# Performance work log

Measured on AMD Instinct MI355X. Metric: run time of the kernel, lower is better.

The kernel has to match this reference:

```python
import jax, jax.numpy as jnp
import numpy as np

EMB = 128
EA = 32
ET = 32
N = 50000
E = 500000
EPS = 1e-5
DROP_P = 0.1


def setup_inputs() -> dict:
    key = jax.random.key(0)
    ks = jax.random.split(key, 12)
    din = EMB + EA + ET
    return {
        "hidden": jax.random.normal(ks[0], (N, EMB), jnp.float32),
        "edge_index": jax.random.randint(ks[1], (2, E), 0, N, jnp.int64 if jax.config.jax_enable_x64 else jnp.int32),
        "edge_attr": jax.random.normal(ks[2], (E, EA), jnp.float32),
        "edge_time_emb": jax.random.normal(ks[3], (E, ET), jnp.float32),
        "boundary_condition": jax.random.normal(ks[4], (N, EMB), jnp.float32),
        # learned params (torch Linear stored transposed: [in, out])
        "W_msg": jax.random.normal(ks[5], (din, EMB), jnp.float32) / np.sqrt(din),
        "b_msg": jnp.zeros((EMB,), jnp.float32),
        "W_lin": jax.random.normal(ks[6], (EMB, EMB), jnp.float32) / np.sqrt(EMB),
        "b_lin": jnp.zeros((EMB,), jnp.float32),
        "ln_gamma": jnp.ones((EMB,), jnp.float32),
        "ln_beta": jnp.zeros((EMB,), jnp.float32),
    }


def reference(hidden, edge_index, edge_attr, edge_time_emb, boundary_condition,
              W_msg, b_msg, W_lin, b_lin, ln_gamma, ln_beta):
    num_nodes = hidden.shape[0]
    # gather source node features, concat with edge features -> [E, emb+ea+et]
    msg = jnp.concatenate([hidden[edge_index[0]], edge_attr, edge_time_emb], axis=1)
    msg = jax.nn.relu(msg @ W_msg + b_msg)                      # [E, emb]
    # append boundary condition as self-loop messages
    msg_aug = jnp.concatenate([msg, boundary_condition], axis=0)
    idx_aug = jnp.concatenate([edge_index[1], jnp.arange(num_nodes, dtype=edge_index.dtype)])
    out = jax.ops.segment_sum(msg_aug, idx_aug, num_segments=num_nodes)  # scatter-sum [N, emb]
    out = out @ W_lin + b_lin
    # LayerNorm (eps=1e-5, affine)
    mean = out.mean(-1, keepdims=True)
    var = out.var(-1, keepdims=True)
    out = (out - mean) * jax.lax.rsqrt(var + EPS) * ln_gamma + ln_beta
    out = jax.nn.relu(out)
    # dropout p=0.1, training=True (fixed key for reproducibility)
    keep = jax.random.bernoulli(jax.random.key(42), 1.0 - DROP_P, out.shape)
    out = jnp.where(keep, out / (1.0 - DROP_P), 0.0)
    return out
```

## Files before the change

### kernel.cpp

```cpp
#include <hip/hip_runtime.h>
#include <stdint.h>

#define NN 50000
#define NE 500000
#define SPB 32
#define NEB (NE / SPB)
#define NT_BLOCKS ((NN + 63) / 64)
#define DEG_STRIDE (NT_BLOCKS * 256)
#define NBLK_N ((NN + 255) / 256)

typedef short bf16x8 __attribute__((ext_vector_type(8)));
typedef float f32x4 __attribute__((ext_vector_type(4)));
typedef unsigned short u16;
typedef unsigned short u16x4 __attribute__((ext_vector_type(4)));
typedef unsigned short u16x8 __attribute__((ext_vector_type(8)));
typedef unsigned int u32x2 __attribute__((ext_vector_type(2)));
typedef unsigned int u32x4 __attribute__((ext_vector_type(4)));

__device__ __forceinline__ u16 f2b(float x) {
  uint32_t u = __builtin_bit_cast(uint32_t, x);
  return (u16)((u + 0x7fffu + ((u >> 16) & 1u)) >> 16);
}
__device__ __forceinline__ float b2f(uint32_t lo16) {
  return __builtin_bit_cast(float, lo16 << 16);
}

__device__ __forceinline__ void threefry(uint32_t x0, uint32_t x1,
                                         uint32_t& o0, uint32_t& o1) {
  const uint32_t k0 = 0u, k1 = 42u, k2 = 0u ^ 42u ^ 0x1BD11BDAu;
  x0 += k0; x1 += k1;
#define TFR(r) { x0 += x1; x1 = (x1 << r) | (x1 >> (32 - r)); x1 ^= x0; }
  TFR(13) TFR(15) TFR(26) TFR(6)
  x0 += k1; x1 += k2 + 1u;
  TFR(17) TFR(29) TFR(16) TFR(24)
  x0 += k2; x1 += k0 + 2u;
  TFR(13) TFR(15) TFR(26) TFR(6)
  x0 += k0; x1 += k1 + 3u;
  TFR(17) TFR(29) TFR(16) TFR(24)
  x0 += k1; x1 += k2 + 4u;
  TFR(13) TFR(15) TFR(26) TFR(6)
  x0 += k2; x1 += k0 + 5u;
#undef TFR
  o0 = x0; o1 = x1;
}

__device__ __forceinline__ bool jax_keep(uint32_t j) {
  uint32_t o0, o1;
  threefry(0u, j, o0, o1);
  uint32_t bits = o0 ^ o1;
  float u = __builtin_bit_cast(float, (bits >> 9) | 0x3f800000u) - 1.0f;
  return u < 0.9f;
}

__global__ __launch_bounds__(256) void k_prep(const float* __restrict__ Wmsg,
                                              const float* __restrict__ Wlin,
                                              u16* __restrict__ WhImg,
                                              u16* __restrict__ WcImg,
                                              u16* __restrict__ WlImg,
                                              uint32_t* __restrict__ deg) {
  const int t = threadIdx.x, b = blockIdx.x;
  if (b == 0) {
#pragma unroll
    for (int it = 0; it < 16; ++it) {
      int g = t + (it << 8);
      int d = g >> 5, k4 = (g & 31) << 2;
      u16x4 v = {f2b(Wmsg[(k4 + 0) * 128 + d]), f2b(Wmsg[(k4 + 1) * 128 + d]),
                 f2b(Wmsg[(k4 + 2) * 128 + d]), f2b(Wmsg[(k4 + 3) * 128 + d])};
      *(u16x4*)&WhImg[(d << 7) + k4] = v;
    }
  } else if (b == 1) {
#pragma unroll
    for (int it = 0; it < 8; ++it) {
      int g = t + (it << 8);
      int d = g >> 4, k4 = (g & 15) << 2;
      u16x4 v = {f2b(Wmsg[(128 + k4 + 0) * 128 + d]), f2b(Wmsg[(128 + k4 + 1) * 128 + d]),
                 f2b(Wmsg[(128 + k4 + 2) * 128 + d]), f2b(Wmsg[(128 + k4 + 3) * 128 + d])};
      *(u16x4*)&WcImg[(d << 6) + k4] = v;
    }
  } else if (b == 2) {
#pragma unroll
    for (int it = 0; it < 16; ++it) {
      int g = t + (it << 8);
      int d = g >> 5, k4 = (g & 31) << 2;
      u16x4 v = {f2b(Wlin[(k4 + 0) * 128 + d]), f2b(Wlin[(k4 + 1) * 128 + d]),
                 f2b(Wlin[(k4 + 2) * 128 + d]), f2b(Wlin[(k4 + 3) * 128 + d])};
      *(u16x4*)&WlImg[(d << 7) + k4] = v;
    }
  } else {
    for (int i = ((b - 3) << 8) + t; i < NN; i += 13 * 256) deg[i] = 0u;
  }
}

__global__ __launch_bounds__(256) void k_scan1(const uint32_t* __restrict__ deg,
                                               uint32_t* __restrict__ ex,
                                               uint32_t* __restrict__ bsum) {
  __shared__ uint32_t s[256];
  int t = threadIdx.x;
  int i = blockIdx.x * 256 + t;
  uint32_t v = (i < NN) ? deg[i] : 0u;
  s[t] = v;
  __syncthreads();
#pragma unroll
  for (int off = 1; off < 256; off <<= 1) {
    uint32_t y = (t >= off) ? s[t - off] : 0u;
    __syncthreads();
    s[t] += y;
    __syncthreads();
  }
  if (i < NN) ex[i] = s[t] - v;
  if (t == 255) bsum[blockIdx.x] = s[255];
}

__global__ __launch_bounds__(256) void k_scan23(const uint32_t* __restrict__ bsum,
                                                const uint32_t* __restrict__ ex,
                                                uint32_t* __restrict__ cursor) {
  __shared__ uint32_t s[256];
  int t = threadIdx.x;
  uint32_t v = (t < NBLK_N) ? bsum[t] : 0u;
  s[t] = v;
  __syncthreads();
#pragma unroll
  for (int off = 1; off < 256; off <<= 1) {
    uint32_t y = (t >= off) ? s[t - off] : 0u;
    __syncthreads();
    s[t] += y;
    __syncthreads();
  }
  const uint32_t boff = s[blockIdx.x] - bsum[blockIdx.x];
  int i = blockIdx.x * 256 + t;
  if (i < NN) cursor[i] = ex[i] + boff;
}

__global__ __launch_bounds__(256) void k_perm(const int* __restrict__ ei,
                                              uint32_t* __restrict__ cursor,
                                              u32x2* __restrict__ psd) {
  int i = blockIdx.x * 256 + threadIdx.x;
  if (i < NE) {
    uint32_t s = (uint32_t)ei[i], d = (uint32_t)ei[NE + i];
    uint32_t pos = atomicAdd(&cursor[d], 1u);
    u32x2 pv = {(uint32_t)i, s | (d << 16)};
    psd[pos] = pv;
  }
}

__global__ __launch_bounds__(256, 8) void k_edge3(const u32x2* __restrict__ psd,
                                                  const float* __restrict__ attr,
                                                  const float* __restrict__ tim,
                                                  const u16* __restrict__ WcImg,
                                                  const u16* __restrict__ Hp,
                                                  float* __restrict__ acc) {
  __shared__ union { u16 A[32 * 64]; float C[32 * 128]; } lds;
  __shared__ int sdst[32];
  const int t = threadIdx.x;
  const long e0 = (long)blockIdx.x << 5;

  const int row = t >> 3, g = t & 7;
  const u32x2 pv = psd[e0 + row];
  const int e = (int)pv.x;
  const int src = (int)(pv.y & 0xffffu);
  const float* src8 = (g < 4) ? (attr + ((size_t)e << 5) + (g << 3))
                              : (tim + ((size_t)e << 5) + ((g - 4) << 3));
  f32x4 v0 = *(const f32x4*)src8;
  f32x4 v1 = *(const f32x4*)(src8 + 4);
  u16x8 bb = {f2b(v0[0]), f2b(v0[1]), f2b(v0[2]), f2b(v0[3]),
              f2b(v1[0]), f2b(v1[1]), f2b(v1[2]), f2b(v1[3])};
  *(u16x8*)&lds.A[(row << 6) + ((g ^ (row & 7)) << 3)] = bb;
  const u32x4 hpA = *(const u32x4*)(Hp + ((size_t)src << 7) + (g << 4));
  const u32x4 hpB = *(const u32x4*)(Hp + ((size_t)src << 7) + (g << 4) + 8);
  if (g == 0) sdst[row] = (int)(pv.y >> 16);
  __syncthreads();

  const int lane = t & 63, w = t >> 6;
  const int quad = lane >> 4, lr = lane & 15;
  f32x4 c[2][2];
#pragma unroll
  for (int i = 0; i < 2; ++i)
#pragma unroll
    for (int j = 0; j < 2; ++j) { f32x4 z = {0.f, 0.f, 0.f, 0.f}; c[i][j] = z; }
#pragma unroll
  for (int ks = 0; ks < 64; ks += 32) {
    const int gi = (ks >> 3) + quad;
    bf16x8 a[2], b[2];
#pragma unroll
    for (int i = 0; i < 2; ++i) {
      int r2 = (i << 4) + lr;
      a[i] = *(const bf16x8*)&lds.A[(r2 << 6) + ((gi ^ (r2 & 7)) << 3)];
    }
#pragma unroll
    for (int j = 0; j < 2; ++j) {
      int col = (w << 5) + (j << 4) + lr;
      b[j] = *(const bf16x8*)&WcImg[(col << 6) + (gi << 3)];
    }
#pragma unroll
    for (int i = 0; i < 2; ++i)
#pragma unroll
      for (int j = 0; j < 2; ++j)
        c[i][j] = __builtin_amdgcn_mfma_f32_16x16x32_bf16(a[i], b[j], c[i][j], 0, 0, 0);
  }
  __syncthreads();
#pragma unroll
  for (int i = 0; i < 2; ++i)
#pragma unroll
    for (int j = 0; j < 2; ++j)
#pragma unroll
      for (int r = 0; r < 4; ++r) {
        int rr = (i << 4) + (quad << 2) + r;
        int col = (w << 5) + (j << 4) + lr;
        lds.C[(rr << 7) + ((((col >> 2) ^ rr) << 2) + (col & 3))] = c[i][j][r];
      }
  __syncthreads();
  {
#pragma unroll
    for (int gg = 0; gg < 4; ++gg) {
      int cb4 = (g << 2) + gg;
      float* p = &lds.C[(row << 7) + ((cb4 ^ row) << 2)];
      f32x4 cv = *(const f32x4*)p;
      const u32x4 hw = (gg < 2) ? hpA : hpB;
      const int k = (gg & 1) << 1;
      uint32_t w0 = hw[k], w1 = hw[k + 1];
      cv[0] = fmaxf(cv[0] + b2f(w0 & 0xffffu), 0.f);
      cv[1] = fmaxf(cv[1] + b2f(w0 >> 16), 0.f);
      cv[2] = fmaxf(cv[2] + b2f(w1 & 0xffffu), 0.f);
      cv[3] = fmaxf(cv[3] + b2f(w1 >> 16), 0.f);
      *(f32x4*)p = cv;
    }
  }
  __syncthreads();
  {
    const int col = t & 127, half = t >> 7;
    const int beg = half << 4, end = beg + 16;
    int cur = sdst[beg];
    float sum = 0.f;
    int runstart = beg;
    for (int ss = beg; ss < end; ++ss) {
      int d = sdst[ss];
      if (d != cur) {
        if (cur >= 0) {
          float* p = acc + ((size_t)cur << 7) + col;
          if (runstart == beg) unsafeAtomicAdd(p, sum);
          else *p = sum;
        }
        cur = d; sum = 0.f; runstart = ss;
      }
      sum += lds.C[(ss << 7) + ((((col >> 2) ^ ss) << 2) + (col & 3))];
    }
    if (cur >= 0) unsafeAtomicAdd(acc + ((size_t)cur << 7) + col, sum);
  }
}

__global__ __launch_bounds__(256) void k_hp(const float* __restrict__ hidden,
                                            const u16* __restrict__ WhImg,
                                            const float* __restrict__ bmsg,
                                            const int* __restrict__ ei,
                                            uint32_t* __restrict__ deg,
                                            u16* __restrict__ Hp,
                                            float* __restrict__ acc) {
  __shared__ u16 sA[64 * 128];
  const int t = threadIdx.x;
  const int row0 = blockIdx.x << 6;
  {
    f32x4* acc4 = (f32x4*)acc;
    const f32x4 z = {0.f, 0.f, 0.f, 0.f};
    for (int i = blockIdx.x * 256 + t; i < NN * 32; i += DEG_STRIDE) acc4[i] = z;
  }
  for (int i = blockIdx.x * 256 + t; i < NE; i += DEG_STRIDE)
    atomicAdd(&deg[ei[NE + i]], 1u);
#pragma unroll
  for (int it = 0; it < 8; ++it) {
    int li = t + (it << 8);
    int row = li >> 5, c4 = li & 31;
    int n = row0 + row;
    f32x4 v = {0.f, 0.f, 0.f, 0.f};
    if (n < NN) v = *(const f32x4*)(hidden + ((size_t)n << 7) + (c4 << 2));
    u16x4 b = {f2b(v[0]), f2b(v[1]), f2b(v[2]), f2b(v[3])};
    *(u16x4*)&sA[(row << 7) + ((((c4 >> 1) ^ (row & 15)) << 3) + ((c4 & 1) << 2))] = b;
  }
  __syncthreads();
  const int lane = t & 63, w = t >> 6;
  const int quad = lane >> 4, lr = lane & 15;
  f32x4 c[4][2];
#pragma unroll
  for (int i = 0; i < 4; ++i)
#pragma unroll
    for (int j = 0; j < 2; ++j) { f32x4 z = {0.f, 0.f, 0.f, 0.f}; c[i][j] = z; }
#pragma unroll
  for (int ks = 0; ks < 128; ks += 32) {
    const int gi = (ks >> 3) + quad;
    bf16x8 a[4], b[2];
#pragma unroll
    for (int i = 0; i < 4; ++i) {
      int row = (i << 4) + lr;
      a[i] = *(const bf16x8*)&sA[(row << 7) + ((gi ^ (row & 15)) << 3)];
    }
#pragma unroll
    for (int j = 0; j < 2; ++j) {
      int col = (w << 5) + (j << 4) + lr;
      b[j] = *(const bf16x8*)&WhImg[(col << 7) + (gi << 3)];
    }
#pragma unroll
    for (int i = 0; i < 4; ++i)
#pragma unroll
      for (int j = 0; j < 2; ++j)
        c[i][j] = __builtin_amdgcn_mfma_f32_16x16x32_bf16(a[i], b[j], c[i][j], 0, 0, 0);
  }
#pragma unroll
  for (int j = 0; j < 2; ++j) {
    int d = (w << 5) + (j << 4) + lr;
    float bias = bmsg[d];
#pragma unroll
    for (int i = 0; i < 4; ++i) {
      int nb = row0 + (i << 4) + (quad << 2);
#pragma unroll
      for (int r = 0; r < 4; ++r) {
        int n = nb + r;
        if (n < NN) Hp[((size_t)n << 7) + d] = f2b(c[i][j][r] + bias);
      }
    }
  }
}

__global__ __launch_bounds__(256) void k_out(float* accout,
                                             const float* __restrict__ bnd,
                                             const u16* __restrict__ WlImg,
                                             const float* __restrict__ blin,
                                             const float* __restrict__ gam,
                                             const float* __restrict__ bet) {
  __shared__ union { u16 A[64 * 128]; float C[64 * 128]; } lds;
  const int t = threadIdx.x;
  const int row0 = blockIdx.x << 6;
#pragma unroll
  for (int it = 0; it < 8; ++it) {
    int li = t + (it << 8);
    int row = li >> 5, c4 = li & 31;
    int n = row0 + row;
    f32x4 v = {0.f, 0.f, 0.f, 0.f};
    if (n < NN) {
      f32x4 a = *(const f32x4*)(accout + ((size_t)n << 7) + (c4 << 2));
      f32x4 b = *(const f32x4*)(bnd + ((size_t)n << 7) + (c4 << 2));
      v = a + b;
    }
    u16x4 bb = {f2b(v[0]), f2b(v[1]), f2b(v[2]), f2b(v[3])};
    *(u16x4*)&lds.A[(row << 7) + ((((c4 >> 1) ^ (row & 15)) << 3) + ((c4 & 1) << 2))] = bb;
  }
  __syncthreads();
  const int lane = t & 63, w = t >> 6;
  const int quad = lane >> 4, lr = lane & 15;
  f32x4 c[4][2];
#pragma unroll
  for (int i = 0; i < 4; ++i)
#pragma unroll
    for (int j = 0; j < 2; ++j) { f32x4 z = {0.f, 0.f, 0.f, 0.f}; c[i][j] = z; }
#pragma unroll
  for (int ks = 0; ks < 128; ks += 32) {
    const int gi = (ks >> 3) + quad;
    bf16x8 a[4], b[2];
#pragma unroll
    for (int i = 0; i < 4; ++i) {
      int row = (i << 4) + lr;
      a[i] = *(const bf16x8*)&lds.A[(row << 7) + ((gi ^ (row & 15)) << 3)];
    }
#pragma unroll
    for (int j = 0; j < 2; ++j) {
      int col = (w << 5) + (j << 4) + lr;
      b[j] = *(const bf16x8*)&WlImg[(col << 7) + (gi << 3)];
    }
#pragma unroll
    for (int i = 0; i < 4; ++i)
#pragma unroll
      for (int j = 0; j < 2; ++j)
        c[i][j] = __builtin_amdgcn_mfma_f32_16x16x32_bf16(a[i], b[j], c[i][j], 0, 0, 0);
  }
  __syncthreads();
#pragma unroll
  for (int i = 0; i < 4; ++i)
#pragma unroll
    for (int j = 0; j < 2; ++j)
#pragma unroll
      for (int r = 0; r < 4; ++r) {
        int row = (i << 4) + (quad << 2) + r;
        int col = (w << 5) + (j << 4) + lr;
        lds.C[(row << 7) + ((((col >> 2) ^ (row & 31)) << 2) + (col & 3))] = c[i][j][r];
      }
  __syncthreads();
  const int row = t >> 2, q = t & 3;
  const int n = row0 + row;
  float s1 = 0.f, s2 = 0.f;
  if (n < NN) {
#pragma unroll
    for (int g = 0; g < 8; ++g) {
      int g5 = (q << 3) + g;
      f32x4 cv = *(const f32x4*)&lds.C[(row << 7) + ((g5 ^ (row & 31)) << 2)];
      f32x4 bl = *(const f32x4*)(blin + (g5 << 2));
#pragma unroll
      for (int m = 0; m < 4; ++m) {
        float x = cv[m] + bl[m];
        s1 += x; s2 += x * x;
      }
    }
  }
  s1 += __shfl_xor(s1, 1, 64); s1 += __shfl_xor(s1, 2, 64);
  s2 += __shfl_xor(s2, 1, 64); s2 += __shfl_xor(s2, 2, 64);
  if (n < NN) {
    const float mean = s1 * 0.0078125f;
    const float var = s2 * 0.0078125f - mean * mean;
    const float inv = 1.0f / sqrtf(var + 1e-5f);
#pragma unroll
    for (int g = 0; g < 8; ++g) {
      int g5 = (q << 3) + g;
      int d0 = g5 << 2;
      f32x4 cv = *(const f32x4*)&lds.C[(row << 7) + ((g5 ^ (row & 31)) << 2)];
      f32x4 bl = *(const f32x4*)(blin + d0);
      f32x4 gm = *(const f32x4*)(gam + d0);
      f32x4 bb = *(const f32x4*)(bet + d0);
      f32x4 o;
#pragma unroll
      for (int m = 0; m < 4; ++m) {
        float x = cv[m] + bl[m];
        float y = fmaxf((x - mean) * inv * gm[m] + bb[m], 0.f);
        uint32_t jj = ((uint32_t)n << 7) + (uint32_t)(d0 + m);
        o[m] = jax_keep(jj) ? (y * (1.0f / 0.9f)) : 0.0f;
      }
      *(f32x4*)(accout + ((size_t)n << 7) + d0) = o;
    }
  }
}

extern "C" void kernel_launch(void* const* d_in, const int* in_sizes, int n_in,
                              void* d_out, int out_size, void* d_ws, size_t ws_size,
                              hipStream_t stream) {
  (void)in_sizes; (void)n_in; (void)out_size; (void)ws_size;
  const float* hidden = (const float*)d_in[0];
  const int*   ei     = (const int*)d_in[1];
  const float* attr   = (const float*)d_in[2];
  const float* tim    = (const float*)d_in[3];
  const float* bnd    = (const float*)d_in[4];
  const float* Wmsg   = (const float*)d_in[5];
  const float* bmsg   = (const float*)d_in[6];
  const float* Wlin   = (const float*)d_in[7];
  const float* blin   = (const float*)d_in[8];
  const float* gam    = (const float*)d_in[9];
  const float* bet    = (const float*)d_in[10];

  float* acc = (float*)d_out;

  char* ws = (char*)d_ws;
  u16*      Hp     = (u16*)(ws + 0);
  u16*      WhImg  = (u16*)(ws + 12800000);
  u16*      WcImg  = (u16*)(ws + 12832768);
  u16*      WlImg  = (u16*)(ws + 12849152);
  uint32_t* deg    = (uint32_t*)(ws + 12881920);
  uint32_t* cursor = (uint32_t*)(ws + 13081920);
  uint32_t* bsum   = (uint32_t*)(ws + 13281920);
  uint32_t* ex     = (uint32_t*)(ws + 13282944);
  u32x2*    psd    = (u32x2*)(ws + 13482944);

  k_prep  <<<dim3(16), dim3(256), 0, stream>>>(Wmsg, Wlin, WhImg, WcImg, WlImg, deg);
  k_hp    <<<dim3(NT_BLOCKS), dim3(256), 0, stream>>>(hidden, WhImg, bmsg, ei, deg, Hp, acc);
  k_scan1 <<<dim3(NBLK_N), dim3(256), 0, stream>>>(deg, ex, bsum);
  k_scan23<<<dim3(NBLK_N), dim3(256), 0, stream>>>(bsum, ex, cursor);
  k_perm  <<<dim3((NE + 255) / 256), dim3(256), 0, stream>>>(ei, cursor, psd);
  k_edge3 <<<dim3(NEB), dim3(256), 0, stream>>>(psd, attr, tim, WcImg, Hp, acc);
  k_out   <<<dim3(NT_BLOCKS), dim3(256), 0, stream>>>(acc, bnd, WlImg, blin, gam, bet);
}
```

Before: 332.7 us.

## Shrink node-GEMM tiles to 16 rows and stage outputs through LDS for coalesced stores

k_hp and k_out now process 16 nodes per block instead of 64, giving 3125 blocks, and each thread loads and converts 8 contiguous floats. Results pass through a swizzled LDS buffer so Hp and the final output are written as coalesced 16-byte vectors rather than scattered 2-byte stores. The degree-count loop becomes one edge per thread, and the LayerNorm reduction spans 16 lanes per row. The intent is more parallelism and better store coalescing on the node-level kernels. The cost is that each block reloads the weight matrix for only 16 rows, so weight reuse per block drops. Bounds checks are removed, which relies on N being a multiple of 16.

```diff
diff --git a/kernel.cpp b/kernel.cpp
--- a/kernel.cpp
+++ b/kernel.cpp
@@ -5,8 +5,8 @@
 #define NE 500000
 #define SPB 32
 #define NEB (NE / SPB)
-#define NT_BLOCKS ((NN + 63) / 64)
-#define DEG_STRIDE (NT_BLOCKS * 256)
+#define NT16 3125
+#define ST16 (NT16 * 256)
 #define NBLK_N ((NN + 255) / 256)
 
 typedef short bf16x8 __attribute__((ext_vector_type(8)));
@@ -255,67 +255,64 @@
                                             uint32_t* __restrict__ deg,
                                             u16* __restrict__ Hp,
                                             float* __restrict__ acc) {
-  __shared__ u16 sA[64 * 128];
+  __shared__ union { u16 A[16 * 128]; float C[16 * 128]; } lds;
   const int t = threadIdx.x;
-  const int row0 = blockIdx.x << 6;
+  const int row0 = blockIdx.x << 4;
   {
     f32x4* acc4 = (f32x4*)acc;
     const f32x4 z = {0.f, 0.f, 0.f, 0.f};
-    for (int i = blockIdx.x * 256 + t; i < NN * 32; i += DEG_STRIDE) acc4[i] = z;
-  }
-  for (int i = blockIdx.x * 256 + t; i < NE; i += DEG_STRIDE)
-    atomicAdd(&deg[ei[NE + i]], 1u);
-#pragma unroll
-  for (int it = 0; it < 8; ++it) {
-    int li = t + (it << 8);
-    int row = li >> 5, c4 = li & 31;
-    int n = row0 + row;
-    f32x4 v = {0.f, 0.f, 0.f, 0.f};
-    if (n < NN) v = *(const f32x4*)(hidden + ((size_t)n << 7) + (c4 << 2));
-    u16x4 b = {f2b(v[0]), f2b(v[1]), f2b(v[2]), f2b(v[3])};
-    *(u16x4*)&sA[(row << 7) + ((((c4 >> 1) ^ (row & 15)) << 3) + ((c4 & 1) << 2))] = b;
+    for (int i = blockIdx.x * 256 + t; i < NN * 32; i += ST16) acc4[i] = z;
+  }
+  {
+    int i = blockIdx.x * 256 + t;
+    if (i < NE) atomicAdd(&deg[ei[NE + i]], 1u);
+  }
+  const int srow = t >> 4, sq = t & 15;
+  {
+    const float* hp8 = hidden + ((size_t)(row0 + srow) << 7) + (sq << 3);
+    f32x4 v0 = *(const f32x4*)hp8;
+    f32x4 v1 = *(const f32x4*)(hp8 + 4);
+    u16x8 b = {f2b(v0[0]), f2b(v0[1]), f2b(v0[2]), f2b(v0[3]),
+               f2b(v1[0]), f2b(v1[1]), f2b(v1[2]), f2b(v1[3])};
+    *(u16x8*)&lds.A[(srow << 7) + ((sq ^ srow) << 3)] = b;
   }
   __syncthreads();
   const int lane = t & 63, w = t >> 6;
   const int quad = lane >> 4, lr = lane & 15;
-  f32x4 c[4][2];
-#pragma unroll
-  for (int i = 0; i < 4; ++i)
-#pragma unroll
-    for (int j = 0; j < 2; ++j) { f32x4 z = {0.f, 0.f, 0.f, 0.f}; c[i][j] = z; }
+  f32x4 c[2];
+#pragma unroll
+  for (int j = 0; j < 2; ++j) { f32x4 z = {0.f, 0.f, 0.f, 0.f}; c[j] = z; }
 #pragma unroll
   for (int ks = 0; ks < 128; ks += 32) {
     const int gi = (ks >> 3) + quad;
-    bf16x8 a[4], b[2];
-#pragma unroll
-    for (int i = 0; i < 4; ++i) {
-      int row = (i << 4) + lr;
-      a[i] = *(const bf16x8*)&sA[(row << 7) + ((gi ^ (row & 15)) << 3)];
-    }
+    bf16x8 a = *(const bf16x8*)&lds.A[(lr << 7) + ((gi ^ lr) << 3)];
 #pragma unroll
     for (int j = 0; j < 2; ++j) {
       int col = (w << 5) + (j << 4) + lr;
-      b[j] = *(const bf16x8*)&WhImg[(col << 7) + (gi << 3)];
-    }
-#pragma unroll
-    for (int i = 0; i < 4; ++i)
-#pragma unroll
-      for (int j = 0; j < 2; ++j)
-        c[i][j] = __builtin_amdgcn_mfma_f32_16x16x32_bf16(a[i], b[j], c[i][j], 0, 0, 0);
-  }
+      bf16x8 b = *(const bf16x8*)&WhImg[(col << 7) + (gi << 3)];
+      c[j] = __builtin_amdgcn_mfma_f32_16x16x32_bf16(a, b, c[j], 0, 0, 0);
+    }
+  }
+  __syncthreads();
 #pragma unroll
   for (int j = 0; j < 2; ++j) {
-    int d = (w << 5) + (j << 4) + lr;
-    float bias = bmsg[d];
-#pragma unroll
-    for (int i = 0; i < 4; ++i) {
-      int nb = row0 + (i << 4) + (quad << 2);
-#pragma unroll
-      for (int r = 0; r < 4; ++r) {
-        int n = nb + r;
-        if (n < NN) Hp[((size_t)n << 7) + d] = f2b(c[i][j][r] + bias);
-      }
-    }
+    int col = (w << 5) + (j << 4) + lr;
+    float bias = bmsg[col];
+    int g4 = col >> 2;
+#pragma unroll
+    for (int r = 0; r < 4; ++r) {
+      int rr = (quad << 2) + r;
+      lds.C[(rr << 7) + (((g4 ^ (rr & 7)) << 2) + (col & 3))] = c[j][r] + bias;
+    }
+  }
+  __syncthreads();
+  {
+    const f32x4* C4 = (const f32x4*)lds.C;
+    f32x4 v0 = C4[(srow << 5) + (((sq << 1) | 0) ^ (srow & 7))];
+    f32x4 v1 = C4[(srow << 5) + (((sq << 1) | 1) ^ (srow & 7))];
+    u16x8 b = {f2b(v0[0]), f2b(v0[1]), f2b(v0[2]), f2b(v0[3]),
+               f2b(v1[0]), f2b(v1[1]), f2b(v1[2]), f2b(v1[3])};
+    *(u16x8*)&Hp[((size_t)(row0 + srow) << 7) + (sq << 3)] = b;
   }
 }
 
@@ -325,104 +322,82 @@
                                              const float* __restrict__ blin,
                                              const float* __restrict__ gam,
                                              const float* __restrict__ bet) {
-  __shared__ union { u16 A[64 * 128]; float C[64 * 128]; } lds;
+  __shared__ union { u16 A[16 * 128]; float C[16 * 128]; } lds;
   const int t = threadIdx.x;
-  const int row0 = blockIdx.x << 6;
-#pragma unroll
-  for (int it = 0; it < 8; ++it) {
-    int li = t + (it << 8);
-    int row = li >> 5, c4 = li & 31;
-    int n = row0 + row;
-    f32x4 v = {0.f, 0.f, 0.f, 0.f};
-    if (n < NN) {
-      f32x4 a = *(const f32x4*)(accout + ((size_t)n << 7) + (c4 << 2));
-      f32x4 b = *(const f32x4*)(bnd + ((size_t)n << 7) + (c4 << 2));
-      v = a + b;
-    }
-    u16x4 bb = {f2b(v[0]), f2b(v[1]), f2b(v[2]), f2b(v[3])};
-    *(u16x4*)&lds.A[(row << 7) + ((((c4 >> 1) ^ (row & 15)) << 3) + ((c4 & 1) << 2))] = bb;
+  const int row0 = blockIdx.x << 4;
+  const int srow = t >> 4, sq = t & 15;
+  const int n = row0 + srow;
+  {
+    const float* ap = accout + ((size_t)n << 7) + (sq << 3);
+    const float* bp = bnd + ((size_t)n << 7) + (sq << 3);
+    f32x4 a0 = *(const f32x4*)ap, a1 = *(const f32x4*)(ap + 4);
+    f32x4 b0 = *(const f32x4*)bp, b1 = *(const f32x4*)(bp + 4);
+    f32x4 v0 = a0 + b0, v1 = a1 + b1;
+    u16x8 b = {f2b(v0[0]), f2b(v0[1]), f2b(v0[2]), f2b(v0[3]),
+               f2b(v1[0]), f2b(v1[1]), f2b(v1[2]), f2b(v1[3])};
+    *(u16x8*)&lds.A[(srow << 7) + ((sq ^ srow) << 3)] = b;
   }
   __syncthreads();
   const int lane = t & 63, w = t >> 6;
   const int quad = lane >> 4, lr = lane & 15;
-  f32x4 c[4][2];
-#pragma unroll
-  for (int i = 0; i < 4; ++i)
-#pragma unroll
-    for (int j = 0; j < 2; ++j) { f32x4 z = {0.f, 0.f, 0.f, 0.f}; c[i][j] = z; }
+  f32x4 c[2];
+#pragma unroll
+  for (int j = 0; j < 2; ++j) { f32x4 z = {0.f, 0.f, 0.f, 0.f}; c[j] = z; }
 #pragma unroll
   for (int ks = 0; ks < 128; ks += 32) {
     const int gi = (ks >> 3) + quad;
-    bf16x8 a[4], b[2];
-#pragma unroll
-    for (int i = 0; i < 4; ++i) {
-      int row = (i << 4) + lr;
-      a[i] = *(const bf16x8*)&lds.A[(row << 7) + ((gi ^ (row & 15)) << 3)];
-    }
+    bf16x8 a = *(const bf16x8*)&lds.A[(lr << 7) + ((gi ^ lr) << 3)];
 #pragma unroll
     for (int j = 0; j < 2; ++j) {
       int col = (w << 5) + (j << 4) + lr;
-      b[j] = *(const bf16x8*)&WlImg[(col << 7) + (gi << 3)];
-    }
-#pragma unroll
-    for (int i = 0; i < 4; ++i)
-#pragma unroll
-      for (int j = 0; j < 2; ++j)
-        c[i][j] = __builtin_amdgcn_mfma_f32_16x16x32_bf16(a[i], b[j], c[i][j], 0, 0, 0);
-  }
-  __syncthreads();
-#pragma unroll
-  for (int i = 0; i < 4; ++i)
-#pragma unroll
-    for (int j = 0; j < 2; ++j)
-#pragma unroll
-      for (int r = 0; r < 4; ++r) {
-        int row = (i << 4) + (quad << 2) + r;
-        int col = (w << 5) + (j << 4) + lr;
-        lds.C[(row << 7) + ((((col >> 2) ^ (row & 31)) << 2) + (col & 3))] = c[i][j][r];
-      }
-  __syncthreads();
-  const int row = t >> 2, q = t & 3;
-  const int n = row0 + row;
+      bf16x8 b = *(const bf16x8*)&WlImg[(col << 7) + (gi << 3)];
+      c[j] = __builtin_amdgcn_mfma_f32_16x16x32_bf16(a, b, c[j], 0, 0, 0);
+    }
+  }
+  __syncthreads();
+#pragma unroll
+  for (int j = 0; j < 2; ++j) {
+    int col = (w << 5) + (j << 4) + lr;
+    float bias = blin[col];
+    int g4 = col >> 2;
+#pragma unroll
+    for (int r = 0; r < 4; ++r) {
+      int rr = (quad << 2) + r;
+      lds.C[(rr << 7) + (((g4 ^ (rr & 7)) << 2) + (col & 3))] = c[j][r] + bias;
+    }
+  }
+  __syncthreads();
+  const f32x4* C4 = (const f32x4*)lds.C;
+  f32x4 x0 = C4[(srow << 5) + (((sq << 1) | 0) ^ (srow & 7))];
+  f32x4 x1 = C4[(srow << 5) + (((sq << 1) | 1) ^ (srow & 7))];
   float s1 = 0.f, s2 = 0.f;
-  if (n < NN) {
-#pragma unroll
-    for (int g = 0; g < 8; ++g) {
-      int g5 = (q << 3) + g;
-      f32x4 cv = *(const f32x4*)&lds.C[(row << 7) + ((g5 ^ (row & 31)) << 2)];
-      f32x4 bl = *(const f32x4*)(blin + (g5 << 2));
-#pragma unroll
-      for (int m = 0; m < 4; ++m) {
-        float x = cv[m] + bl[m];
-        s1 += x; s2 += x * x;
-      }
-    }
+#pragma unroll
+  for (int m = 0; m < 4; ++m) {
+    s1 += x0[m] + x1[m];
+    s2 += x0[m] * x0[m] + x1[m] * x1[m];
   }
   s1 += __shfl_xor(s1, 1, 64); s1 += __shfl_xor(s1, 2, 64);
+  s1 += __shfl_xor(s1, 4, 64); s1 += __shfl_xor(s1, 8, 64);
   s2 += __shfl_xor(s2, 1, 64); s2 += __shfl_xor(s2, 2, 64);
-  if (n < NN) {
-    const float mean = s1 * 0.0078125f;
-    const float var = s2 * 0.0078125f - mean * mean;
-    const float inv = 1.0f / sqrtf(var + 1e-5f);
-#pragma unroll
-    for (int g = 0; g < 8; ++g) {
-      int g5 = (q << 3) + g;
-      int d0 = g5 << 2;
-      f32x4 cv = *(const f32x4*)&lds.C[(row << 7) + ((g5 ^ (row & 31)) << 2)];
-      f32x4 bl = *(const f32x4*)(blin + d0);
-      f32x4 gm = *(const f32x4*)(gam + d0);
-      f32x4 bb = *(const f32x4*)(bet + d0);
-      f32x4 o;
-#pragma unroll
-      for (int m = 0; m < 4; ++m) {
-        float x = cv[m] + bl[m];
-        float y = fmaxf((x - mean) * inv * gm[m] + bb[m], 0.f);
-        uint32_t jj = ((uint32_t)n << 7) + (uint32_t)(d0 + m);
-        o[m] = jax_keep(jj) ? (y * (1.0f / 0.9f)) : 0.0f;
-      }
-      *(f32x4*)(accout + ((size_t)n << 7) + d0) = o;
-    }
-  }
+  s2 += __shfl_xor(s2, 4, 64); s2 += __shfl_xor(s2, 8, 64);
+  const float mean = s1 * 0.0078125f;
+  const float var = s2 * 0.0078125f - mean * mean;
+  const float inv = 1.0f / sqrtf(var + 1e-5f);
+  const int d0 = sq << 3;
+  f32x4 gm0 = *(const f32x4*)(gam + d0), gm1 = *(const f32x4*)(gam + d0 + 4);
+  f32x4 bb0 = *(const f32x4*)(bet + d0), bb1 = *(const f32x4*)(bet + d0 + 4);
+  f32x4 o0, o1;
+#pragma unroll
+  for (int m = 0; m < 4; ++m) {
+    float y0 = fmaxf((x0[m] - mean) * inv * gm0[m] + bb0[m], 0.f);
+    float y1 = fmaxf((x1[m] - mean) * inv * gm1[m] + bb1[m], 0.f);
+    uint32_t j0 = ((uint32_t)n << 7) + (uint32_t)(d0 + m);
+    uint32_t j1 = j0 + 4u;
+    o0[m] = jax_keep(j0) ? (y0 * (1.0f / 0.9f)) : 0.0f;
+    o1[m] = jax_keep(j1) ? (y1 * (1.0f / 0.9f)) : 0.0f;
+  }
+  *(f32x4*)(accout + ((size_t)n << 7) + d0) = o0;
+  *(f32x4*)(accout + ((size_t)n << 7) + d0 + 4) = o1;
 }
 
 extern "C" void kernel_launch(void* const* d_in, const int* in_sizes, int n_in,
@@ -455,10 +430,10 @@
   u32x2*    psd    = (u32x2*)(ws + 13482944);
 
   k_prep  <<<dim3(16), dim3(256), 0, stream>>>(Wmsg, Wlin, WhImg, WcImg, WlImg, deg);
-  k_hp    <<<dim3(NT_BLOCKS), dim3(256), 0, stream>>>(hidden, WhImg, bmsg, ei, deg, Hp, acc);
+  k_hp    <<<dim3(NT16), dim3(256), 0, stream>>>(hidden, WhImg, bmsg, ei, deg, Hp, acc);
   k_scan1 <<<dim3(NBLK_N), dim3(256), 0, stream>>>(deg, ex, bsum);
   k_scan23<<<dim3(NBLK_N), dim3(256), 0, stream>>>(bsum, ex, cursor);
   k_perm  <<<dim3((NE + 255) / 256), dim3(256), 0, stream>>>(ei, cursor, psd);
   k_edge3 <<<dim3(NEB), dim3(256), 0, stream>>>(psd, attr, tim, WcImg, Hp, acc);
-  k_out   <<<dim3(NT_BLOCKS), dim3(256), 0, stream>>>(acc, bnd, WlImg, blin, gam, bet);
-}
+  k_out   <<<dim3(NT16), dim3(256), 0, stream>>>(acc, bnd, WlImg, blin, gam, bet);
+}
```

Result: no change. 330.2 us (-0.7%).
